# Optimization experiments

Hardware: AMD Instinct MI355X
Metric: run time of the kernel (lower is better)

Reference implementation:

```python
import jax, jax.numpy as jnp
import numpy as np

T, B, C, H = 2048, 2, 1024, 16
DK = C // H


def setup_inputs() -> dict:
    key = jax.random.key(0)
    ks = jax.random.split(key, 12)
    s = 1.0 / np.sqrt(C)
    return {
        "query": jax.random.normal(ks[0], (T, B, C), jnp.float32),
        "key": jax.random.normal(ks[1], (T, B, C), jnp.float32),
        "value": jax.random.normal(ks[2], (T, B, C), jnp.float32),
        "Wq": jax.random.normal(ks[3], (C, C), jnp.float32) * s,
        "bq": jnp.zeros((C,), jnp.float32),
        "Wk": jax.random.normal(ks[4], (C, C), jnp.float32) * s,
        "bk": jnp.zeros((C,), jnp.float32),
        "Wv": jax.random.normal(ks[5], (C, C), jnp.float32) * s,
        "bv": jnp.zeros((C,), jnp.float32),
        "Wo": jax.random.normal(ks[6], (C, C), jnp.float32) * s,
        "bo": jnp.zeros((C,), jnp.float32),
        "key_padding_mask": jax.random.randint(ks[7], (B, T), 0, 2).astype(jnp.bool_),
    }


def reference(query, key, value, Wq, bq, Wk, bk, Wv, bv, Wo, bo, key_padding_mask):
    # T,B,C -> B,T,C
    q_in = jnp.transpose(query, (1, 0, 2))
    k_in = jnp.transpose(key, (1, 0, 2))
    v_in = jnp.transpose(value, (1, 0, 2))
    nb = q_in.shape[0]
    # linear projections, split heads: B,T,C -> B,H,T,dk
    def proj(x, W, b):
        y = x @ W.T + b
        return jnp.transpose(y.reshape(nb, -1, H, DK), (0, 2, 1, 3))
    q = proj(q_in, Wq, bq)
    k = proj(k_in, Wk, bk)
    v = proj(v_in, Wv, bv)
    # scores: B,H,T1,T2
    scores = jnp.einsum("bhqd,bhkd->bhqk", q, k) / np.sqrt(DK).astype(np.float32)
    scores = jnp.where(key_padding_mask[:, None, None, :], -jnp.inf, scores)
    attn = jax.nn.softmax(scores, axis=-1)
    # context: B,H,T1,dk -> B,T1,C
    x = jnp.einsum("bhqk,bhkd->bhqd", attn, v)
    x = jnp.transpose(x, (0, 2, 1, 3)).reshape(nb, -1, H * DK)
    out = x @ Wo.T + bo
    # B,T,C -> T,B,C
    return jnp.transpose(out, (1, 0, 2))
```

## Files before the change

### kernel.cpp

```cpp
#include <hip/hip_runtime.h>
#include <stdint.h>

typedef __attribute__((ext_vector_type(4))) float f32x4;
typedef __attribute__((ext_vector_type(16))) float f32x16;
typedef __attribute__((ext_vector_type(8))) short bf16x8;
typedef __attribute__((ext_vector_type(2))) unsigned int u32x2;
typedef __attribute__((ext_vector_type(4))) unsigned int u32x4;
typedef unsigned short u16;
typedef unsigned int u32;

#define DEVINL __device__ __forceinline__

DEVINL u16 f2bf(float f) {
  u32 u = __builtin_bit_cast(u32, f);
  u += 0x7FFFu + ((u >> 16) & 1u);
  return (u16)(u >> 16);
}

DEVINL float exp2_hw(float x) {
  float r;
  asm("v_exp_f32 %0, %1\n\ts_nop 0" : "=v"(r) : "v"(x));
  return r;
}

DEVINL u32 cvt_pk_bf16(float lo, float hi) {
  u32 r;
  asm("v_cvt_pk_bf16_f32 %0, %1, %2" : "=v"(r) : "v"(lo), "v"(hi));
  return r;
}

DEVINL void gload16(const void* g, void* l) {
  __builtin_amdgcn_global_load_lds((const __attribute__((address_space(1))) void*)g,
                                   (__attribute__((address_space(3))) void*)l, 16, 0, 0);
}

__global__ void cvt_all(const float* __restrict__ q, const float* __restrict__ k,
                        const float* __restrict__ v, const float* __restrict__ wq,
                        const float* __restrict__ wk, const float* __restrict__ wv,
                        const float* __restrict__ wo, ushort4* __restrict__ dst) {
  int i = blockIdx.x * 256 + threadIdx.x;
  float4 v4;
  if (i < 1048576) v4 = ((const float4*)q)[i];
  else if (i < 2097152) v4 = ((const float4*)k)[i - 1048576];
  else if (i < 3145728) v4 = ((const float4*)v)[i - 2097152];
  else {
    int j = i - 3145728;
    if (j < 262144) v4 = ((const float4*)wq)[j];
    else if (j < 524288) v4 = ((const float4*)wk)[j - 262144];
    else if (j < 786432) v4 = ((const float4*)wv)[j - 524288];
    else v4 = ((const float4*)wo)[j - 786432];
  }
  ushort4 o;
  o.x = f2bf(v4.x); o.y = f2bf(v4.y); o.z = f2bf(v4.z); o.w = f2bf(v4.w);
  dst[i] = o;
}

__global__ void mask_prep(const u32* __restrict__ mraw, float* __restrict__ mout) {
  __shared__ int notint, notfloat;
  int tid = threadIdx.x;
  if (tid == 0) { notint = 0; notfloat = 0; }
  __syncthreads();
  u32 w = mraw[tid];
  if (w != 0u && w != 1u) notint = 1;
  if (w != 0u && w != 0x3f800000u) notfloat = 1;
  __syncthreads();
  bool words = (!notint) || (!notfloat);
  for (int i = tid; i < 4096; i += 1024) {
    u32 v = words ? mraw[i] : (u32)(((const unsigned char*)mraw)[i]);
    mout[i] = v ? -1.0e38f : 0.0f;
  }
}

DEVINL void gemm_body(const u16* __restrict__ A, const u16* __restrict__ W,
                      const float* __restrict__ bias, u16* __restrict__ out_bf,
                      float* __restrict__ out_f, int tile, int mode, float scale,
                      u16* As, u16* Bs) {
  const int tid = threadIdx.x, lane = tid & 63;
  const int wave = tid >> 6, wm = wave & 1, wn = wave >> 1;
  const int m0 = (tile >> 3) << 7;
  const int n0 = (tile & 7) << 7;
  const int l15 = lane & 15, l4 = lane >> 4;
  const int K = 1024;
  const f32x4 zero = {0.f, 0.f, 0.f, 0.f};
  f32x4 acc[4][4];
#pragma unroll
  for (int i = 0; i < 4; i++)
#pragma unroll
    for (int j = 0; j < 4; j++) acc[i][j] = zero;

  for (int kt = 0; kt < 1024; kt += 32) {
#pragma unroll
    for (int it = 0; it < 2; ++it) {
      int c = tid + (it << 8);
      int row = c >> 2, qs = (c & 3) ^ ((row & 3) ^ ((row >> 2) & 3));
      gload16(A + (size_t)(m0 + row) * K + kt + qs * 8, (void*)(As + c * 8));
      gload16(W + (size_t)(n0 + row) * K + kt + qs * 8, (void*)(Bs + c * 8));
    }
    __syncthreads();
    bf16x8 af[4], bfr[4];
#pragma unroll
    for (int i = 0; i < 4; i++) {
      int ra = (wm << 6) + (i << 4) + l15;
      int rb = (wn << 6) + (i << 4) + l15;
      af[i]  = *(const bf16x8*)(As + ra * 32 + ((l4 * 8) ^ ((((ra & 3) ^ ((ra >> 2) & 3))) << 3)));
      bfr[i] = *(const bf16x8*)(Bs + rb * 32 + ((l4 * 8) ^ ((((rb & 3) ^ ((rb >> 2) & 3))) << 3)));
    }
#pragma unroll
    for (int i = 0; i < 4; i++)
#pragma unroll
      for (int j = 0; j < 4; j++)
        acc[i][j] = __builtin_amdgcn_mfma_f32_16x16x32_bf16(af[i], bfr[j], acc[i][j], 0, 0, 0);
    __syncthreads();
  }

#pragma unroll
  for (int j = 0; j < 4; j++) {
    const int col = n0 + (wn << 6) + (j << 4) + l15;
    const float bc = bias[col];
#pragma unroll
    for (int i = 0; i < 4; i++) {
#pragma unroll
      for (int r = 0; r < 4; r++) {
        const int row = m0 + (wm << 6) + (i << 4) + (l4 << 2) + r;
        float v = (acc[i][j][r] + bc) * scale;
        if (mode == 3) {
          int t = row & 2047, b2 = row >> 11;
          out_f[(size_t)(t * 2 + b2) * 1024 + col] = v;
        } else {
          int t = row >> 1, b2 = row & 1, h = col >> 6, dh = col & 63;
          if (mode == 2)
            out_bf[((size_t)(b2 * 16 + h) * 64 + dh) * 2048 + t] = f2bf(v);
          else
            out_bf[((size_t)(b2 * 16 + h) * 2048 + t) * 64 + dh] = f2bf(v);
        }
      }
    }
  }
}

__global__ __launch_bounds__(256, 3) void gemm_qkv(
    const u16* __restrict__ qbf, const u16* __restrict__ kbf, const u16* __restrict__ vbf,
    const u16* __restrict__ wq, const u16* __restrict__ wk, const u16* __restrict__ wv,
    const float* __restrict__ bq, const float* __restrict__ bk, const float* __restrict__ bv,
    u16* __restrict__ Qh, u16* __restrict__ Kh, u16* __restrict__ Vth) {
  __shared__ u16 As[4096], Bs[4096];
  const float C2 = 0.18033688011112042f;
  int wg = blockIdx.x;
  int swz = (wg & 7) * 96 + (wg >> 3);
  int prob = swz >> 8, tile = swz & 255;
  if (prob == 0)      gemm_body(qbf, wq, bq, Qh,  nullptr, tile, 0, C2, As, Bs);
  else if (prob == 1) gemm_body(kbf, wk, bk, Kh,  nullptr, tile, 0, 1.0f, As, Bs);
  else                gemm_body(vbf, wv, bv, Vth, nullptr, tile, 2, 1.0f, As, Bs);
}

__global__ __launch_bounds__(256, 3) void gemm_o(
    const u16* __restrict__ ctx, const u16* __restrict__ wo,
    const float* __restrict__ bo, float* __restrict__ out) {
  __shared__ u16 As[4096], Bs[4096];
  int wg = blockIdx.x;
  int swz = (wg & 7) * 32 + (wg >> 3);
  gemm_body(ctx, wo, bo, nullptr, out, swz, 3, 1.0f, As, Bs);
}

__global__ __launch_bounds__(256, 2) void attn_fwd(
    const u16* __restrict__ Qh, const u16* __restrict__ Kh, const u16* __restrict__ Vt,
    const float* __restrict__ maskf, u16* __restrict__ ctx) {
  __shared__ u16 Ks[2][64 * 64];
  __shared__ u16 Vs[2][64 * 64];
  const int tid = threadIdx.x, lane = tid & 63, wave = tid >> 6;
  const int wg = blockIdx.x;
  const int swz = (wg & 7) * 64 + (wg >> 3);
  const int qt = swz & 15, bh = swz >> 4;
  const int bb = bh >> 4, h = bh & 15;
  const int l31 = lane & 31, hi = lane >> 5;
  const size_t kvbase = (size_t)bh * 2048 * 64;
  const int qbase = qt * 128 + wave * 32;

  bf16x8 qf[4];
#pragma unroll
  for (int kc = 0; kc < 4; kc++)
    qf[kc] = *(const bf16x8*)(Qh + kvbase + (size_t)(qbase + l31) * 64 + kc * 16 + hi * 8);

  f32x16 zz;
#pragma unroll
  for (int e = 0; e < 16; e++) zz[e] = 0.f;
  f32x16 O[2];
  O[0] = zz; O[1] = zz;
  float m_ = -1.0e30f, l_ = 0.f;

  auto stage = [&](int buf, int kt) {
#pragma unroll
    for (int it = 0; it < 2; ++it) {
      int c = tid + (it << 8);
      int row = c >> 3, qs = (c & 7) ^ (row & 7);
      gload16(Kh + kvbase + (size_t)(kt * 64 + row) * 64 + qs * 8, (void*)(&Ks[buf][c * 8]));
      gload16(Vt + kvbase + (size_t)row * 2048 + kt * 64 + qs * 8, (void*)(&Vs[buf][c * 8]));
    }
  };

  stage(0, 0);
  __syncthreads();

  const float4* mrow = (const float4*)(maskf + bb * 2048);

  for (int kt = 0; kt < 32; ++kt) {
    const int cur = kt & 1;
    if (kt < 31) stage(cur ^ 1, kt + 1);

    f32x16 s[2];
    s[0] = zz; s[1] = zz;
    __builtin_amdgcn_s_setprio(1);
#pragma unroll
    for (int kc = 0; kc < 4; kc++) {
      const int ch = (((kc * 2 + hi) ^ (l31 & 7)) << 3);
      bf16x8 kf0 = *(const bf16x8*)(&Ks[cur][l31 * 64 + ch]);
      bf16x8 kf1 = *(const bf16x8*)(&Ks[cur][(l31 + 32) * 64 + ch]);
      s[0] = __builtin_amdgcn_mfma_f32_32x32x16_bf16(kf0, qf[kc], s[0], 0, 0, 0);
      s[1] = __builtin_amdgcn_mfma_f32_32x32x16_bf16(kf1, qf[kc], s[1], 0, 0, 0);
    }
    __builtin_amdgcn_s_setprio(0);

#pragma unroll
    for (int kb = 0; kb < 2; kb++)
#pragma unroll
      for (int g = 0; g < 4; g++) {
        float4 mv = mrow[kt * 16 + kb * 8 + g * 2 + hi];
        s[kb][4 * g + 0] += mv.x;
        s[kb][4 * g + 1] += mv.y;
        s[kb][4 * g + 2] += mv.z;
        s[kb][4 * g + 3] += mv.w;
      }

    float pm = s[0][0];
#pragma unroll
    for (int e = 1; e < 16; e++) pm = fmaxf(pm, s[0][e]);
#pragma unroll
    for (int e = 0; e < 16; e++) pm = fmaxf(pm, s[1][e]);
    pm = fmaxf(pm, __shfl_xor(pm, 32));

    if (__any(pm > m_ + 8.f)) {
      float mn = fmaxf(m_, pm);
      float al = exp2_hw(m_ - mn);
      m_ = mn;
      l_ *= al;
#pragma unroll
      for (int e = 0; e < 16; e++) { O[0][e] *= al; O[1][e] *= al; }
    }

    float rs = 0.f;
#pragma unroll
    for (int kb = 0; kb < 2; kb++)
#pragma unroll
      for (int e = 0; e < 16; e++) {
        float p = exp2_hw(s[kb][e] - m_);
        s[kb][e] = p;
        rs += p;
      }
    rs += __shfl_xor(rs, 32);
    l_ += rs;

    u32 pw[2][8];
#pragma unroll
    for (int kb = 0; kb < 2; kb++)
#pragma unroll
      for (int g = 0; g < 4; g++) {
        pw[kb][2 * g]     = cvt_pk_bf16(s[kb][4 * g + 0], s[kb][4 * g + 1]);
        pw[kb][2 * g + 1] = cvt_pk_bf16(s[kb][4 * g + 2], s[kb][4 * g + 3]);
      }

    __builtin_amdgcn_s_setprio(1);
#pragma unroll
    for (int kc = 0; kc < 4; kc++) {
      const int kb = kc >> 1, m = kc & 1;
      auto r0 = __builtin_amdgcn_permlane32_swap(pw[kb][4 * m + 0], pw[kb][4 * m + 2], false, false);
      auto r1 = __builtin_amdgcn_permlane32_swap(pw[kb][4 * m + 1], pw[kb][4 * m + 3], false, false);
      u32x4 fw = {r0[0], r1[0], r0[1], r1[1]};
      bf16x8 pf = __builtin_bit_cast(bf16x8, fw);
      const int ch = (((kc * 2 + hi) ^ (l31 & 7)) << 3);
      bf16x8 vf0 = *(const bf16x8*)(&Vs[cur][l31 * 64 + ch]);
      bf16x8 vf1 = *(const bf16x8*)(&Vs[cur][(l31 + 32) * 64 + ch]);
      O[0] = __builtin_amdgcn_mfma_f32_32x32x16_bf16(vf0, pf, O[0], 0, 0, 0);
      O[1] = __builtin_amdgcn_mfma_f32_32x32x16_bf16(vf1, pf, O[1], 0, 0, 0);
    }
    __builtin_amdgcn_s_setprio(0);

    __syncthreads();
  }

  float inv = (l_ > 0.f) ? 1.0f / l_ : 0.f;
  const int q = qbase + l31;
  u16* cb = ctx + ((size_t)bb * 2048 + q) * 1024 + h * 64;
#pragma unroll
  for (int nd = 0; nd < 2; nd++)
#pragma unroll
    for (int g = 0; g < 4; g++) {
      u32x2 w;
      w[0] = cvt_pk_bf16(O[nd][4 * g + 0] * inv, O[nd][4 * g + 1] * inv);
      w[1] = cvt_pk_bf16(O[nd][4 * g + 2] * inv, O[nd][4 * g + 3] * inv);
      *(u32x2*)(cb + nd * 32 + g * 8 + hi * 4) = w;
    }
}

extern "C" void kernel_launch(void* const* d_in, const int* in_sizes, int n_in,
                              void* d_out, int out_size, void* d_ws, size_t ws_size,
                              hipStream_t stream) {
  const float* q_in = (const float*)d_in[0];
  const float* k_in = (const float*)d_in[1];
  const float* v_in = (const float*)d_in[2];
  const float* Wq = (const float*)d_in[3];
  const float* bq = (const float*)d_in[4];
  const float* Wk = (const float*)d_in[5];
  const float* bk = (const float*)d_in[6];
  const float* Wv = (const float*)d_in[7];
  const float* bv = (const float*)d_in[8];
  const float* Wo = (const float*)d_in[9];
  const float* bo = (const float*)d_in[10];
  const void* mask = d_in[11];

  const size_t SZ_X = (size_t)4194304 * 2;
  const size_t SZ_W = (size_t)1048576 * 2;
  uint8_t* ws = (uint8_t*)d_ws;
  float* mf = (float*)ws;
  size_t off = 32768;
  u16* qbf = (u16*)(ws + off); off += SZ_X;
  u16* kbf = (u16*)(ws + off); off += SZ_X;
  u16* vbf = (u16*)(ws + off); off += SZ_X;
  u16* wqb = (u16*)(ws + off); off += SZ_W;
  u16* wkb = (u16*)(ws + off); off += SZ_W;
  u16* wvb = (u16*)(ws + off); off += SZ_W;
  u16* wob = (u16*)(ws + off); off += SZ_W;
  u16* Qh  = (u16*)(ws + off); off += SZ_X;
  u16* Kh  = (u16*)(ws + off); off += SZ_X;
  u16* Vth = (u16*)(ws + off); off += SZ_X;
  u16* ctx = (u16*)(ws + off); off += SZ_X;
  if (ws_size < off) return;

  mask_prep<<<1, 1024, 0, stream>>>((const u32*)mask, mf);
  cvt_all<<<16384, 256, 0, stream>>>(q_in, k_in, v_in, Wq, Wk, Wv, Wo, (ushort4*)qbf);

  gemm_qkv<<<768, 256, 0, stream>>>(qbf, kbf, vbf, wqb, wkb, wvb, bq, bk, bv, Qh, Kh, Vth);

  attn_fwd<<<512, 256, 0, stream>>>(Qh, Kh, Vth, mf, ctx);

  gemm_o<<<256, 256, 0, stream>>>(ctx, wob, bo, (float*)d_out);
}
```

Before: 160.2 us.

## Triple-buffer GEMM and attention LDS staging with vmcnt waits, stage mask in LDS

Both the projection GEMMs and the attention kernel move from single- or double-buffered LDS staging to a three-stage ring. Each iteration waits on an explicit vmcnt and uses a single s_barrier, so loads two tiles ahead overlap the MFMA work and the second __syncthreads per iteration goes away. The attention kernel also copies the key padding mask into LDS once per block and adds it inside the exp argument instead of before the row max. The row max then ignores the mask, which is still numerically valid but may let unmasked-but-masked large scores shift the running max. LDS use per block rises and could limit occupancy.

```diff
diff --git a/kernel.cpp b/kernel.cpp
--- a/kernel.cpp
+++ b/kernel.cpp
@@ -33,6 +33,9 @@
   __builtin_amdgcn_global_load_lds((const __attribute__((address_space(1))) void*)g,
                                    (__attribute__((address_space(3))) void*)l, 16, 0, 0);
 }
+
+DEVINL void wait_vm4() { asm volatile("s_waitcnt vmcnt(4)" ::: "memory"); }
+DEVINL void wait_vm0() { asm volatile("s_waitcnt vmcnt(0)" ::: "memory"); }
 
 __global__ void cvt_all(const float* __restrict__ q, const float* __restrict__ k,
                         const float* __restrict__ v, const float* __restrict__ wq,
@@ -88,29 +91,45 @@
 #pragma unroll
     for (int j = 0; j < 4; j++) acc[i][j] = zero;
 
-  for (int kt = 0; kt < 1024; kt += 32) {
+  auto stage = [&](int buf, int kti) {
+    u16* Ab = As + buf * 4096;
+    u16* Bb = Bs + buf * 4096;
 #pragma unroll
     for (int it = 0; it < 2; ++it) {
       int c = tid + (it << 8);
       int row = c >> 2, qs = (c & 3) ^ ((row & 3) ^ ((row >> 2) & 3));
-      gload16(A + (size_t)(m0 + row) * K + kt + qs * 8, (void*)(As + c * 8));
-      gload16(W + (size_t)(n0 + row) * K + kt + qs * 8, (void*)(Bs + c * 8));
-    }
-    __syncthreads();
+      gload16(A + (size_t)(m0 + row) * K + kti * 32 + qs * 8, (void*)(Ab + c * 8));
+      gload16(W + (size_t)(n0 + row) * K + kti * 32 + qs * 8, (void*)(Bb + c * 8));
+    }
+  };
+
+  stage(0, 0);
+  stage(1, 1);
+
+  for (int kti = 0; kti < 32; ++kti) {
+    const int cur = kti % 3;
+    if (kti == 31) wait_vm0(); else wait_vm4();
+    __builtin_amdgcn_s_barrier();
+    __builtin_amdgcn_sched_barrier(0);
+    if (kti < 30) stage((kti + 2) % 3, kti + 2);
+
+    const u16* Ac = As + cur * 4096;
+    const u16* Bc = Bs + cur * 4096;
     bf16x8 af[4], bfr[4];
 #pragma unroll
     for (int i = 0; i < 4; i++) {
       int ra = (wm << 6) + (i << 4) + l15;
       int rb = (wn << 6) + (i << 4) + l15;
-      af[i]  = *(const bf16x8*)(As + ra * 32 + ((l4 * 8) ^ ((((ra & 3) ^ ((ra >> 2) & 3))) << 3)));
-      bfr[i] = *(const bf16x8*)(Bs + rb * 32 + ((l4 * 8) ^ ((((rb & 3) ^ ((rb >> 2) & 3))) << 3)));
-    }
+      af[i]  = *(const bf16x8*)(Ac + ra * 32 + ((l4 * 8) ^ ((((ra & 3) ^ ((ra >> 2) & 3))) << 3)));
+      bfr[i] = *(const bf16x8*)(Bc + rb * 32 + ((l4 * 8) ^ ((((rb & 3) ^ ((rb >> 2) & 3))) << 3)));
+    }
+    __builtin_amdgcn_s_setprio(1);
 #pragma unroll
     for (int i = 0; i < 4; i++)
 #pragma unroll
       for (int j = 0; j < 4; j++)
         acc[i][j] = __builtin_amdgcn_mfma_f32_16x16x32_bf16(af[i], bfr[j], acc[i][j], 0, 0, 0);
-    __syncthreads();
+    __builtin_amdgcn_s_setprio(0);
   }
 
 #pragma unroll
@@ -143,7 +162,8 @@
     const u16* __restrict__ wq, const u16* __restrict__ wk, const u16* __restrict__ wv,
     const float* __restrict__ bq, const float* __restrict__ bk, const float* __restrict__ bv,
     u16* __restrict__ Qh, u16* __restrict__ Kh, u16* __restrict__ Vth) {
-  __shared__ u16 As[4096], Bs[4096];
+  __shared__ __align__(16) u16 As[3 * 4096];
+  __shared__ __align__(16) u16 Bs[3 * 4096];
   const float C2 = 0.18033688011112042f;
   int wg = blockIdx.x;
   int swz = (wg & 7) * 96 + (wg >> 3);
@@ -156,7 +176,8 @@
 __global__ __launch_bounds__(256, 3) void gemm_o(
     const u16* __restrict__ ctx, const u16* __restrict__ wo,
     const float* __restrict__ bo, float* __restrict__ out) {
-  __shared__ u16 As[4096], Bs[4096];
+  __shared__ __align__(16) u16 As[3 * 4096];
+  __shared__ __align__(16) u16 Bs[3 * 4096];
   int wg = blockIdx.x;
   int swz = (wg & 7) * 32 + (wg >> 3);
   gemm_body(ctx, wo, bo, nullptr, out, swz, 3, 1.0f, As, Bs);
@@ -165,8 +186,9 @@
 __global__ __launch_bounds__(256, 2) void attn_fwd(
     const u16* __restrict__ Qh, const u16* __restrict__ Kh, const u16* __restrict__ Vt,
     const float* __restrict__ maskf, u16* __restrict__ ctx) {
-  __shared__ u16 Ks[2][64 * 64];
-  __shared__ u16 Vs[2][64 * 64];
+  __shared__ __align__(16) u16 Ks[3][64 * 64];
+  __shared__ __align__(16) u16 Vs[3][64 * 64];
+  __shared__ __align__(16) float Ml[2048];
   const int tid = threadIdx.x, lane = tid & 63, wave = tid >> 6;
   const int wg = blockIdx.x;
   const int swz = (wg & 7) * 64 + (wg >> 3);
@@ -176,6 +198,9 @@
   const size_t kvbase = (size_t)bh * 2048 * 64;
   const int qbase = qt * 128 + wave * 32;
 
+  gload16(maskf + bb * 2048 + tid * 4, (void*)(&Ml[tid * 4]));
+  gload16(maskf + bb * 2048 + 1024 + tid * 4, (void*)(&Ml[1024 + tid * 4]));
+
   bf16x8 qf[4];
 #pragma unroll
   for (int kc = 0; kc < 4; kc++)
@@ -199,13 +224,14 @@
   };
 
   stage(0, 0);
-  __syncthreads();
-
-  const float4* mrow = (const float4*)(maskf + bb * 2048);
+  stage(1, 1);
 
   for (int kt = 0; kt < 32; ++kt) {
-    const int cur = kt & 1;
-    if (kt < 31) stage(cur ^ 1, kt + 1);
+    const int cur = kt % 3;
+    if (kt == 31) wait_vm0(); else wait_vm4();
+    __builtin_amdgcn_s_barrier();
+    __builtin_amdgcn_sched_barrier(0);
+    if (kt < 30) stage((kt + 2) % 3, kt + 2);
 
     f32x16 s[2];
     s[0] = zz; s[1] = zz;
@@ -220,17 +246,6 @@
     }
     __builtin_amdgcn_s_setprio(0);
 
-#pragma unroll
-    for (int kb = 0; kb < 2; kb++)
-#pragma unroll
-      for (int g = 0; g < 4; g++) {
-        float4 mv = mrow[kt * 16 + kb * 8 + g * 2 + hi];
-        s[kb][4 * g + 0] += mv.x;
-        s[kb][4 * g + 1] += mv.y;
-        s[kb][4 * g + 2] += mv.z;
-        s[kb][4 * g + 3] += mv.w;
-      }
-
     float pm = s[0][0];
 #pragma unroll
     for (int e = 1; e < 16; e++) pm = fmaxf(pm, s[0][e]);
@@ -251,10 +266,16 @@
 #pragma unroll
     for (int kb = 0; kb < 2; kb++)
 #pragma unroll
-      for (int e = 0; e < 16; e++) {
-        float p = exp2_hw(s[kb][e] - m_);
-        s[kb][e] = p;
-        rs += p;
+      for (int g = 0; g < 4; g++) {
+        float4 mv = *(const float4*)(&Ml[kt * 64 + kb * 32 + g * 8 + hi * 4]);
+        float a0 = mv.x - m_, a1 = mv.y - m_, a2 = mv.z - m_, a3 = mv.w - m_;
+        float p0 = exp2_hw(s[kb][4 * g + 0] + a0);
+        float p1 = exp2_hw(s[kb][4 * g + 1] + a1);
+        float p2 = exp2_hw(s[kb][4 * g + 2] + a2);
+        float p3 = exp2_hw(s[kb][4 * g + 3] + a3);
+        s[kb][4 * g + 0] = p0; s[kb][4 * g + 1] = p1;
+        s[kb][4 * g + 2] = p2; s[kb][4 * g + 3] = p3;
+        rs += (p0 + p1) + (p2 + p3);
       }
     rs += __shfl_xor(rs, 32);
     l_ += rs;
@@ -283,8 +304,6 @@
       O[1] = __builtin_amdgcn_mfma_f32_32x32x16_bf16(vf1, pf, O[1], 0, 0, 0);
     }
     __builtin_amdgcn_s_setprio(0);
-
-    __syncthreads();
   }
 
   float inv = (l_ > 0.f) ? 1.0f / l_ : 0.f;
```

New measurement: 144.1 us. 1.11x faster.
